# Performance work log

Measured on AMD Instinct MI355X. Metric: run time of the kernel, lower is better.

The kernel has to match this reference:

```python
import jax, jax.numpy as jnp
import numpy as np

N_NODES = 100000
N_EDGES = 1600000
NFEAT = 128
NHID = 128
NS = 64
NCLASS = 16
B = 8192


def setup_inputs() -> dict:
    key = jax.random.key(0)
    ks = jax.random.split(key, 12)
    s = jax.random.normal(ks[0], (B, NS), dtype=jnp.float32)
    x = jax.random.normal(ks[1], (N_NODES, NFEAT), dtype=jnp.float32)
    row = jax.random.randint(ks[2], (N_EDGES,), 0, N_NODES)
    col = jax.random.randint(ks[3], (N_EDGES,), 0, N_NODES)
    val = jax.random.uniform(ks[4], (N_EDGES,), dtype=jnp.float32)
    index = jax.random.randint(ks[5], (B,), 0, N_NODES)
    # learned parameters (glorot-ish scale)
    W1 = jax.random.normal(ks[6], (NFEAT, NHID), dtype=jnp.float32) / np.sqrt(NFEAT)
    b1 = jnp.zeros((NHID,), dtype=jnp.float32)
    W2 = jax.random.normal(ks[7], (NHID, NHID), dtype=jnp.float32) / np.sqrt(NHID)
    b2 = jnp.zeros((NHID,), dtype=jnp.float32)
    Wl = jax.random.normal(ks[8], (NHID + NS, NCLASS), dtype=jnp.float32) / np.sqrt(NHID + NS)
    bl = jnp.zeros((NCLASS,), dtype=jnp.float32)
    return {"s": s, "x": x, "row": row, "col": col, "val": val,
            "index": index, "W1": W1, "b1": b1, "W2": W2, "b2": b2,
            "Wl": Wl, "bl": bl}


def reference(s, x, row, col, val, index, W1, b1, W2, b2, Wl, bl):
    n = x.shape[0]

    def spmm(h):
        # adj @ h with adj in COO form: out[r] += val_e * h[c]
        return jax.ops.segment_sum(val[:, None] * h[col], row, num_segments=n)

    # dropout is identity in eval mode (training=False)
    h = jax.nn.relu(spmm(x @ W1) + b1)          # gc1 + relu
    h = spmm(h @ W2) + b2                        # gc2
    z = jnp.concatenate([h[index], s], axis=1) @ Wl + bl  # [B, nclass]
    return jax.nn.log_softmax(z, axis=1)
```

## Files before the change

kernel.cpp:

```cpp
#include <hip/hip_runtime.h>
#include <math.h>

#define N_NODES 100000
#define N_EDGES 1600000
#define NFEAT 128
#define NHID 128
#define NS 64
#define NCLASS 16
#define BB 8192

#define B1_SHIFT 11
#define NB1 49
#define SUB_SHIFT 5
#define NSUB 3125
#define CHUNKA 2048
#define HWG 256
#define BINC_CAP 2048

typedef unsigned long long ull;
typedef unsigned int uint;


__device__ __forceinline__ unsigned short f2bf(float f) {
  unsigned int u = __float_as_uint(f);
  return (unsigned short)((u + 0x7fffu + ((u >> 16) & 1u)) >> 16);
}
__device__ __forceinline__ float bflo(unsigned int u) {
  return __uint_as_float(u << 16);
}
__device__ __forceinline__ float bfhi(unsigned int u) {
  return __uint_as_float(u & 0xffff0000u);
}
__device__ __forceinline__ unsigned int packbf2(float lo, float hi) {
  return (unsigned int)f2bf(lo) | ((unsigned int)f2bf(hi) << 16);
}


__device__ __forceinline__ ull pack_edge(float v, int r, int c) {
  return ((ull)(__float_as_uint(v) >> 2) << 34) | ((ull)(unsigned)r << 17) | (unsigned)c;
}
__device__ __forceinline__ int edge_col(ull p) { return (int)(p & 0x1FFFFu); }
__device__ __forceinline__ int edge_row(ull p) { return (int)((unsigned)(p >> 17) & 0x1FFFFu); }
__device__ __forceinline__ float edge_val(ull p) {
  return __uint_as_float(((unsigned)(p >> 34)) << 2);
}


__global__ __launch_bounds__(256) void selbuild_kernel(const int* __restrict__ index,
                                                       int* __restrict__ sel) {
  int t = blockIdx.x * 256 + threadIdx.x;
  sel[index[t]] = 1;
}

__global__ __launch_bounds__(256) void selflag_kernel(const int* __restrict__ row,
                                                      const int* __restrict__ col,
                                                      const int* __restrict__ sel,
                                                      int* __restrict__ flag) {
  int i = blockIdx.x * blockDim.x + threadIdx.x;
  int stride = gridDim.x * blockDim.x;
  for (; i < N_EDGES; i += stride)
    if (sel[row[i]]) flag[col[i]] = 1;
}

__global__ __launch_bounds__(256) void keepbits_kernel(const int* __restrict__ flag,
                                                       const int* __restrict__ sel,
                                                       uint* __restrict__ keepbits) {
  int t = blockIdx.x * 256 + threadIdx.x;
  if (t >= NSUB) return;
  uint w = 0;
  int base = t * 32;
#pragma unroll
  for (int k = 0; k < 32; ++k) {
    int r = base + k;
    if (r < N_NODES && (flag[r] | sel[r])) w |= (1u << k);
  }
  keepbits[t] = w;
}


__global__ __launch_bounds__(256) void histsub_kernel(const int* __restrict__ row,
                                                      const uint* __restrict__ keepbits,
                                                      int* __restrict__ subcnt) {
  __shared__ int lh[NSUB];
  int tid = threadIdx.x;
  for (int i = tid; i < NSUB; i += 256) lh[i] = 0;
  __syncthreads();
  for (long i = (long)blockIdx.x * 256 + tid; i < N_EDGES; i += (long)HWG * 256) {
    int r = row[i];
    if ((keepbits[r >> 5] >> (r & 31)) & 1u) atomicAdd(&lh[r >> SUB_SHIFT], 1);
  }
  __syncthreads();
  for (int i = tid; i < NSUB; i += 256) {
    int c = lh[i];
    if (c) atomicAdd(&subcnt[i], c);
  }
}


__global__ __launch_bounds__(1024) void scanall_kernel(const int* __restrict__ subcnt,
                                                       int* __restrict__ sub_offs,
                                                       int* __restrict__ gcur1,
                                                       int* __restrict__ gcur2) {
  __shared__ int sd[1024];
  int tid = threadIdx.x;
  int b0 = tid * 4;
  int vv[4];
  int loc = 0;
#pragma unroll
  for (int k = 0; k < 4; ++k) {
    int i = b0 + k;
    vv[k] = (i < NSUB) ? subcnt[i] : 0;
    loc += vv[k];
  }
  sd[tid] = loc;
  __syncthreads();
  for (int o = 1; o < 1024; o <<= 1) {
    int add = (tid >= o) ? sd[tid - o] : 0;
    __syncthreads();
    sd[tid] += add;
    __syncthreads();
  }
  int pre = sd[tid] - loc;
#pragma unroll
  for (int k = 0; k < 4; ++k) {
    int i = b0 + k;
    if (i < NSUB) {
      sub_offs[i] = pre;
      gcur2[i] = pre;
      if ((i & 63) == 0) gcur1[i >> 6] = pre;
      pre += vv[k];
    }
  }
  if (tid == 1023) sub_offs[NSUB] = sd[1023];
}


__global__ __launch_bounds__(256) void binA_kernel(const int* __restrict__ row,
                                                   const int* __restrict__ col,
                                                   const float* __restrict__ val,
                                                   const uint* __restrict__ keepbits,
                                                   int* __restrict__ gcur1,
                                                   ull* __restrict__ ebuf1) {
  __shared__ ull stage[CHUNKA];
  __shared__ short bkt[CHUNKA];
  __shared__ int hist[NB1], lofs[NB1 + 1], lcur[NB1], gbase[NB1];
  int tid = threadIdx.x;
  for (long base = (long)blockIdx.x * CHUNKA; base < N_EDGES; base += (long)gridDim.x * CHUNKA) {
    int cnt = (int)min((long)CHUNKA, (long)N_EDGES - base);
    if (tid < NB1) hist[tid] = 0;
    __syncthreads();
    ull e[8]; int bk[8];
#pragma unroll
    for (int v = 0; v < 8; ++v) {
      int i = v * 256 + tid;
      bk[v] = -1;
      if (i < cnt) {
        long g = base + i;
        int r = row[g];
        if ((keepbits[r >> 5] >> (r & 31)) & 1u) {
          e[v] = pack_edge(val[g], r, col[g]);
          bk[v] = r >> B1_SHIFT;
          atomicAdd(&hist[bk[v]], 1);
        }
      }
    }
    __syncthreads();
    if (tid < 64) {
      int h = (tid < NB1) ? hist[tid] : 0;
      int x = h;
      for (int o = 1; o < 64; o <<= 1) {
        int y = __shfl_up(x, o);
        if (tid >= o) x += y;
      }
      if (tid < NB1) { lofs[tid] = x - h; lcur[tid] = x - h; }
      if (tid == 63) lofs[NB1] = x;
    }
    __syncthreads();
#pragma unroll
    for (int v = 0; v < 8; ++v) {
      if (bk[v] >= 0) {
        int pos = atomicAdd(&lcur[bk[v]], 1);
        stage[pos] = e[v];
        bkt[pos] = (short)bk[v];
      }
    }
    __syncthreads();
    if (tid < NB1) {
      int h = hist[tid];
      if (h > 0) gbase[tid] = atomicAdd(&gcur1[tid], h);
    }
    __syncthreads();
    int tot = lofs[NB1];
    for (int s = tid; s < tot; s += 256) {
      int lo = bkt[s];
      ebuf1[gbase[lo] + (s - lofs[lo])] = stage[s];
    }
    __syncthreads();
  }
}


__global__ __launch_bounds__(256) void binB_kernel(const ull* __restrict__ ebuf1,
                                                   const int* __restrict__ sub_offs,
                                                   int* __restrict__ gcur2,
                                                   ull* __restrict__ edat) {
  __shared__ ull stage[CHUNKA];
  __shared__ short bkt[CHUNKA];
  __shared__ int hist[64], lofs[65], lcur[64], gbase[64];
  int tid = threadIdx.x;
  int b1 = blockIdx.x >> 3, w = blockIdx.x & 7;
  int rbeg = sub_offs[b1 << 6];
  int rend = sub_offs[min((b1 + 1) << 6, NSUB)];
  for (int base = rbeg + w * CHUNKA; base < rend; base += 8 * CHUNKA) {
    int cnt = min(CHUNKA, rend - base);
    if (tid < 64) hist[tid] = 0;
    __syncthreads();
    ull e[8]; int bk[8];
#pragma unroll
    for (int v = 0; v < 8; ++v) {
      int i = v * 256 + tid;
      bk[v] = -1;
      if (i < cnt) {
        e[v] = ebuf1[base + i];
        bk[v] = (edge_row(e[v]) >> SUB_SHIFT) - (b1 << 6);
        atomicAdd(&hist[bk[v]], 1);
      }
    }
    __syncthreads();
    if (tid < 64) {
      int h = hist[tid];
      int x = h;
      for (int o = 1; o < 64; o <<= 1) {
        int y = __shfl_up(x, o);
        if (tid >= o) x += y;
      }
      lofs[tid] = x - h;
      lcur[tid] = x - h;
      if (tid == 63) lofs[64] = x;
    }
    __syncthreads();
#pragma unroll
    for (int v = 0; v < 8; ++v) {
      if (bk[v] >= 0) {
        int pos = atomicAdd(&lcur[bk[v]], 1);
        stage[pos] = e[v];
        bkt[pos] = (short)bk[v];
      }
    }
    __syncthreads();
    if (tid < 64) {
      int h = hist[tid];
      if (h > 0) gbase[tid] = atomicAdd(&gcur2[(b1 << 6) + tid], h);
    }
    __syncthreads();
    for (int s = tid; s < cnt; s += 256) {
      int lo = bkt[s];
      edat[gbase[lo] + (s - lofs[lo])] = stage[s];
    }
    __syncthreads();
  }
}


__global__ __launch_bounds__(256) void binC_kernel(const int* __restrict__ sub_offs,
                                                   ull* __restrict__ edat,
                                                   ull* __restrict__ ebuf1,
                                                   int* __restrict__ offs) {
  __shared__ ull es[BINC_CAP];
  __shared__ int rcnt[32], rcur[32];
  int s = blockIdx.x, tid = threadIdx.x;
  int r0 = s << SUB_SHIFT;
  int beg = sub_offs[s], end = sub_offs[s + 1];
  int n = end - beg;
  if (tid < 32) rcnt[tid] = 0;
  __syncthreads();
  if (n <= BINC_CAP) {
    for (int i = tid; i < n; i += 256) {
      ull p = edat[beg + i];
      es[i] = p;
      atomicAdd(&rcnt[edge_row(p) & 31], 1);
    }
    __syncthreads();
    if (tid < 32) {
      int h = rcnt[tid];
      int x = h;
      for (int o = 1; o < 32; o <<= 1) {
        int y = __shfl_up(x, o, 32);
        if (tid >= o) x += y;
      }
      rcur[tid] = x - h;
      offs[r0 + tid] = beg + x - h;
      if (s == NSUB - 1 && tid == 31) offs[N_NODES] = end;
    }
    __syncthreads();
    for (int i = tid; i < n; i += 256) {
      ull p = es[i];
      int pos = atomicAdd(&rcur[edge_row(p) & 31], 1);
      edat[beg + pos] = p;
    }
  } else {
    for (int i = tid; i < n; i += 256) {
      ull p = edat[beg + i];
      ebuf1[beg + i] = p;
      atomicAdd(&rcnt[edge_row(p) & 31], 1);
    }
    __syncthreads();
    if (tid < 32) {
      int h = rcnt[tid];
      int x = h;
      for (int o = 1; o < 32; o <<= 1) {
        int y = __shfl_up(x, o, 32);
        if (tid >= o) x += y;
      }
      rcur[tid] = x - h;
      offs[r0 + tid] = beg + x - h;
      if (s == NSUB - 1 && tid == 31) offs[N_NODES] = end;
    }
    __syncthreads();
    for (int i = tid; i < n; i += 256) {
      ull p = ebuf1[beg + i];
      int pos = atomicAdd(&rcur[edge_row(p) & 31], 1);
      edat[beg + pos] = p;
    }
  }
}


__global__ __launch_bounds__(256) void wconv2_kernel(const float* __restrict__ W1,
                                                     const float* __restrict__ W2,
                                                     uint* __restrict__ Wt1,
                                                     uint* __restrict__ Wt2) {
  int blk = blockIdx.x;
  const float* W = (blk < 32) ? W1 : W2;
  uint* Wt = (blk < 32) ? Wt1 : Wt2;
  int idx = (blk & 31) * 256 + threadIdx.x;
  int n = idx >> 6, kc = idx & 63;
  float lo = W[(2 * kc) * 128 + n];
  float hi = W[(2 * kc + 1) * 128 + n];
  Wt[idx] = packbf2(lo, hi);
}


typedef __attribute__((ext_vector_type(8))) __bf16 bf16x8;
typedef __attribute__((ext_vector_type(4))) float f32x4;
union FragU { uint4 u; bf16x8 b; };

#define LDSTR 68

template <int OUT_BF16>
__global__ __launch_bounds__(256) void mfma_gemm_kernel(const float* __restrict__ A,
                                                        const uint* __restrict__ Wt_g,
                                                        const float* __restrict__ bias,
                                                        void* __restrict__ C,
                                                        int nrows) {
  __shared__ uint As_s[64 * LDSTR];
  __shared__ uint Wt_s[128 * LDSTR];
  int tid = threadIdx.x;
  int rbase = blockIdx.x * 64;

  {
    const uint2* src = (const uint2*)Wt_g;
#pragma unroll
    for (int i = 0; i < 16; ++i) {
      int j = i * 256 + tid;
      int n = j >> 5, c2 = (j & 31) * 2;
      uint2 v = src[j];
      Wt_s[n * LDSTR + c2] = v.x;
      Wt_s[n * LDSTR + c2 + 1] = v.y;
    }
  }
  {
    const float4* src = (const float4*)(A + (long)rbase * 128);
#pragma unroll
    for (int i = 0; i < 8; ++i) {
      int f = i * 256 + tid;
      int m = f >> 5;
      float4 v = (rbase + m < nrows) ? src[f] : make_float4(0.f, 0.f, 0.f, 0.f);
      int c = (f & 31) * 2;
      As_s[m * LDSTR + c]     = packbf2(v.x, v.y);
      As_s[m * LDSTR + c + 1] = packbf2(v.z, v.w);
    }
  }
  __syncthreads();

  int w = tid >> 6, lane = tid & 63;
  int quad = lane >> 4, lr = lane & 15;
  int n0 = w * 32;

  f32x4 acc[4][2];
#pragma unroll
  for (int mt = 0; mt < 4; ++mt)
#pragma unroll
    for (int nt = 0; nt < 2; ++nt) acc[mt][nt] = (f32x4){0.f, 0.f, 0.f, 0.f};

#pragma unroll
  for (int kk = 0; kk < 4; ++kk) {
    int kc = kk * 16 + quad * 4;
    FragU fb0, fb1;
    fb0.u = *(const uint4*)&Wt_s[(n0 + lr) * LDSTR + kc];
    fb1.u = *(const uint4*)&Wt_s[(n0 + 16 + lr) * LDSTR + kc];
#pragma unroll
    for (int mt = 0; mt < 4; ++mt) {
      FragU fa;
      fa.u = *(const uint4*)&As_s[(mt * 16 + lr) * LDSTR + kc];
      acc[mt][0] = __builtin_amdgcn_mfma_f32_16x16x32_bf16(fa.b, fb0.b, acc[mt][0], 0, 0, 0);
      acc[mt][1] = __builtin_amdgcn_mfma_f32_16x16x32_bf16(fa.b, fb1.b, acc[mt][1], 0, 0, 0);
    }
  }

#pragma unroll
  for (int mt = 0; mt < 4; ++mt) {
#pragma unroll
    for (int nt = 0; nt < 2; ++nt) {
      int col = n0 + nt * 16 + lr;
      float bv = OUT_BF16 ? 0.f : bias[col];
#pragma unroll
      for (int r = 0; r < 4; ++r) {
        int row = rbase + mt * 16 + quad * 4 + r;
        if (row < nrows) {
          if (OUT_BF16)
            ((unsigned short*)C)[(long)row * 128 + col] = f2bf(acc[mt][nt][r]);
          else
            ((float*)C)[(long)row * 128 + col] = acc[mt][nt][r] + bv;
        }
      }
    }
  }
}


__device__ __forceinline__ void fma_row(float* acc, float v, uint4 u) {
  acc[0] = fmaf(v, bflo(u.x), acc[0]);
  acc[1] = fmaf(v, bfhi(u.x), acc[1]);
  acc[2] = fmaf(v, bflo(u.y), acc[2]);
  acc[3] = fmaf(v, bfhi(u.y), acc[3]);
  acc[4] = fmaf(v, bflo(u.z), acc[4]);
  acc[5] = fmaf(v, bfhi(u.z), acc[5]);
  acc[6] = fmaf(v, bflo(u.w), acc[6]);
  acc[7] = fmaf(v, bfhi(u.w), acc[7]);
}

__global__ __launch_bounds__(256) void spmm_row_kernel(const int* __restrict__ offs,
                                                       const ull* __restrict__ edat,
                                                       const unsigned short* __restrict__ a,
                                                       const float* __restrict__ bias,
                                                       unsigned short* __restrict__ h,
                                                       const int* __restrict__ flag) {
  int wave = threadIdx.x >> 6;
  int lane = threadIdx.x & 63;
  int r = blockIdx.x * 4 + wave;
  if (!flag[r]) return;
  int g = lane >> 4, l = lane & 15;
  int s = offs[r], e = offs[r + 1];
  float acc[8] = {0.f, 0.f, 0.f, 0.f, 0.f, 0.f, 0.f, 0.f};
  int j = s + g;
  for (; j + 4 < e; j += 8) {
    ull p0 = edat[j];
    ull p1 = edat[j + 4];
    uint4 u0 = *(const uint4*)(a + (long)edge_col(p0) * 128 + l * 8);
    uint4 u1 = *(const uint4*)(a + (long)edge_col(p1) * 128 + l * 8);
    fma_row(acc, edge_val(p0), u0);
    fma_row(acc, edge_val(p1), u1);
  }
  if (j < e) {
    ull p = edat[j];
    uint4 u = *(const uint4*)(a + (long)edge_col(p) * 128 + l * 8);
    fma_row(acc, edge_val(p), u);
  }
#pragma unroll
  for (int k = 0; k < 8; ++k) {
    acc[k] += __shfl_xor(acc[k], 16);
    acc[k] += __shfl_xor(acc[k], 32);
  }
  if (g == 0) {
    float4 b0 = *(const float4*)(bias + l * 8);
    float4 b1 = *(const float4*)(bias + l * 8 + 4);
    uint4 o;
    o.x = packbf2(fmaxf(acc[0] + b0.x, 0.f), fmaxf(acc[1] + b0.y, 0.f));
    o.y = packbf2(fmaxf(acc[2] + b0.z, 0.f), fmaxf(acc[3] + b0.w, 0.f));
    o.z = packbf2(fmaxf(acc[4] + b1.x, 0.f), fmaxf(acc[5] + b1.y, 0.f));
    o.w = packbf2(fmaxf(acc[6] + b1.z, 0.f), fmaxf(acc[7] + b1.w, 0.f));
    *(uint4*)(h + (long)r * 128 + l * 8) = o;
  }
}

__global__ __launch_bounds__(256) void spmm_sel_kernel(const int* __restrict__ offs,
                                                       const ull* __restrict__ edat,
                                                       const unsigned short* __restrict__ h1,
                                                       const int* __restrict__ index,
                                                       float* __restrict__ g2) {
  int wave = threadIdx.x >> 6;
  int lane = threadIdx.x & 63;
  int b = blockIdx.x * 4 + wave;
  int g = lane >> 4, l = lane & 15;
  int r = index[b];
  int s = offs[r], e = offs[r + 1];
  float acc[8] = {0.f, 0.f, 0.f, 0.f, 0.f, 0.f, 0.f, 0.f};
  int j = s + g;
  for (; j + 4 < e; j += 8) {
    ull p0 = edat[j];
    ull p1 = edat[j + 4];
    uint4 u0 = *(const uint4*)(h1 + (long)edge_col(p0) * 128 + l * 8);
    uint4 u1 = *(const uint4*)(h1 + (long)edge_col(p1) * 128 + l * 8);
    fma_row(acc, edge_val(p0), u0);
    fma_row(acc, edge_val(p1), u1);
  }
  if (j < e) {
    ull p = edat[j];
    uint4 u = *(const uint4*)(h1 + (long)edge_col(p) * 128 + l * 8);
    fma_row(acc, edge_val(p), u);
  }
#pragma unroll
  for (int k = 0; k < 8; ++k) {
    acc[k] += __shfl_xor(acc[k], 16);
    acc[k] += __shfl_xor(acc[k], 32);
  }
  if (g == 0) {
    float* op = g2 + (long)b * 128 + l * 8;
    *(float4*)(op + 0) = make_float4(acc[0], acc[1], acc[2], acc[3]);
    *(float4*)(op + 4) = make_float4(acc[4], acc[5], acc[6], acc[7]);
  }
}


__global__ __launch_bounds__(128) void final_kernel(const float* __restrict__ t,
                                                    const float* __restrict__ s,
                                                    const float* __restrict__ Wl,
                                                    const float* __restrict__ bl,
                                                    float* __restrict__ out) {
  int b = blockIdx.x * 128 + threadIdx.x;
  float z[16];
#pragma unroll
  for (int c = 0; c < 16; ++c) z[c] = bl[c];
  const float4* tb = (const float4*)(t + (long)b * 128);
#pragma unroll 4
  for (int k4 = 0; k4 < 32; ++k4) {
    float4 tv = tb[k4];
    const float* w = Wl + (k4 * 4) * 16;
#pragma unroll
    for (int c = 0; c < 16; ++c)
      z[c] += tv.x * w[c] + tv.y * w[16 + c] + tv.z * w[32 + c] + tv.w * w[48 + c];
  }
  const float4* sb = (const float4*)(s + (long)b * 64);
#pragma unroll 4
  for (int k4 = 0; k4 < 16; ++k4) {
    float4 sv = sb[k4];
    const float* w = Wl + (128 + k4 * 4) * 16;
#pragma unroll
    for (int c = 0; c < 16; ++c)
      z[c] += sv.x * w[c] + sv.y * w[16 + c] + sv.z * w[32 + c] + sv.w * w[48 + c];
  }
  float m = z[0];
#pragma unroll
  for (int c = 1; c < 16; ++c) m = fmaxf(m, z[c]);
  float sum = 0.f;
#pragma unroll
  for (int c = 0; c < 16; ++c) sum += expf(z[c] - m);
  float lse = m + logf(sum);
  float* ob = out + (long)b * 16;
#pragma unroll
  for (int c = 0; c < 16; ++c) ob[c] = z[c] - lse;
}


extern "C" void kernel_launch(void* const* d_in, const int* in_sizes, int n_in,
                              void* d_out, int out_size, void* d_ws, size_t ws_size,
                              hipStream_t stream) {
  const float* s_in  = (const float*)d_in[0];
  const float* x     = (const float*)d_in[1];
  const int*   row   = (const int*)d_in[2];
  const int*   col   = (const int*)d_in[3];
  const float* val   = (const float*)d_in[4];
  const int*   index = (const int*)d_in[5];
  const float* W1    = (const float*)d_in[6];
  const float* b1    = (const float*)d_in[7];
  const float* W2    = (const float*)d_in[8];
  const float* b2    = (const float*)d_in[9];
  const float* Wl    = (const float*)d_in[10];
  const float* bl    = (const float*)d_in[11];
  float* out = (float*)d_out;

  ull* edat  = (ull*)d_ws;
  ull* ebuf1 = edat + N_EDGES;
  unsigned short* a  = (unsigned short*)(ebuf1 + N_EDGES);
  unsigned short* h1 = a + (size_t)N_NODES * 128;
  float* g2   = (float*)(h1 + (size_t)N_NODES * 128);
  float* tmat = g2 + (size_t)BB * 128;
  int* flag   = (int*)(tmat + (size_t)BB * 128);
  int* sel    = flag + N_NODES;
  int* subcnt = sel + N_NODES;
  int* offs   = subcnt + NSUB;
  int* sub_offs = offs + (N_NODES + 1);
  int* gcur1  = sub_offs + (NSUB + 1);
  int* gcur2  = gcur1 + NB1;
  uint* keepbits = (uint*)(gcur2 + NSUB);
  uint* Wt1   = keepbits + NSUB;
  uint* Wt2   = Wt1 + 8192;

  hipMemsetAsync(flag, 0, (2 * N_NODES + NSUB) * sizeof(int), stream);

  selbuild_kernel<<<BB / 256, 256, 0, stream>>>(index, sel);
  selflag_kernel<<<4096, 256, 0, stream>>>(row, col, sel, flag);
  keepbits_kernel<<<(NSUB + 255) / 256, 256, 0, stream>>>(flag, sel, keepbits);

  histsub_kernel<<<HWG, 256, 0, stream>>>(row, keepbits, subcnt);
  scanall_kernel<<<1, 1024, 0, stream>>>(subcnt, sub_offs, gcur1, gcur2);

  binA_kernel<<<512, 256, 0, stream>>>(row, col, val, keepbits, gcur1, ebuf1);
  binB_kernel<<<NB1 * 8, 256, 0, stream>>>(ebuf1, sub_offs, gcur2, edat);
  binC_kernel<<<NSUB, 256, 0, stream>>>(sub_offs, edat, ebuf1, offs);

  wconv2_kernel<<<64, 256, 0, stream>>>(W1, W2, Wt1, Wt2);

  mfma_gemm_kernel<1><<<(N_NODES + 63) / 64, 256, 0, stream>>>(x, Wt1, nullptr, a, N_NODES);
  spmm_row_kernel<<<N_NODES / 4, 256, 0, stream>>>(offs, edat, a, b1, h1, flag);
  spmm_sel_kernel<<<BB / 4, 256, 0, stream>>>(offs, edat, h1, index, g2);
  mfma_gemm_kernel<0><<<BB / 64, 256, 0, stream>>>(g2, Wt2, b2, tmat, BB);
  final_kernel<<<BB / 128, 128, 0, stream>>>(tmat, s_in, Wl, bl, out);
}
```

Before: 307.1 us.

## Build keep bitmask via atomicOr and fuse GEMM2 with final log-softmax layer

Replaces the flag array and keepbits pass with direct atomicOr into a bitmask during selection. Removes the separate weight-conversion kernel by converting W1/W2 to bf16 inside each GEMM block. Fuses the second GEMM with the classifier and log_softmax through shared memory, dropping the intermediate tmat buffer. This removes several launches and a global round-trip, but every GEMM1 block now redundantly reads and converts W1, and spmm_row now also processes selected rows.

```diff
diff --git a/kernel.cpp b/kernel.cpp
--- a/kernel.cpp
+++ b/kernel.cpp
@@ -44,42 +44,36 @@
 __device__ __forceinline__ float edge_val(ull p) {
   return __uint_as_float(((unsigned)(p >> 34)) << 2);
 }
+__device__ __forceinline__ int keep_test(const uint* keep, int r) {
+  return (keep[r >> 5] >> (r & 31)) & 1u;
+}
 
 
 __global__ __launch_bounds__(256) void selbuild_kernel(const int* __restrict__ index,
-                                                       int* __restrict__ sel) {
+                                                       int* __restrict__ sel,
+                                                       uint* __restrict__ keep) {
   int t = blockIdx.x * 256 + threadIdx.x;
-  sel[index[t]] = 1;
+  int r = index[t];
+  sel[r] = 1;
+  atomicOr(&keep[r >> 5], 1u << (r & 31));
 }
 
 __global__ __launch_bounds__(256) void selflag_kernel(const int* __restrict__ row,
                                                       const int* __restrict__ col,
                                                       const int* __restrict__ sel,
-                                                      int* __restrict__ flag) {
+                                                      uint* __restrict__ keep) {
   int i = blockIdx.x * blockDim.x + threadIdx.x;
   int stride = gridDim.x * blockDim.x;
   for (; i < N_EDGES; i += stride)
-    if (sel[row[i]]) flag[col[i]] = 1;
-}
-
-__global__ __launch_bounds__(256) void keepbits_kernel(const int* __restrict__ flag,
-                                                       const int* __restrict__ sel,
-                                                       uint* __restrict__ keepbits) {
-  int t = blockIdx.x * 256 + threadIdx.x;
-  if (t >= NSUB) return;
-  uint w = 0;
-  int base = t * 32;
-#pragma unroll
-  for (int k = 0; k < 32; ++k) {
-    int r = base + k;
-    if (r < N_NODES && (flag[r] | sel[r])) w |= (1u << k);
-  }
-  keepbits[t] = w;
+    if (sel[row[i]]) {
+      int c = col[i];
+      atomicOr(&keep[c >> 5], 1u << (c & 31));
+    }
 }
 
 
 __global__ __launch_bounds__(256) void histsub_kernel(const int* __restrict__ row,
-                                                      const uint* __restrict__ keepbits,
+                                                      const uint* __restrict__ keep,
                                                       int* __restrict__ subcnt) {
   __shared__ int lh[NSUB];
   int tid = threadIdx.x;
@@ -87,7 +81,7 @@
   __syncthreads();
   for (long i = (long)blockIdx.x * 256 + tid; i < N_EDGES; i += (long)HWG * 256) {
     int r = row[i];
-    if ((keepbits[r >> 5] >> (r & 31)) & 1u) atomicAdd(&lh[r >> SUB_SHIFT], 1);
+    if (keep_test(keep, r)) atomicAdd(&lh[r >> SUB_SHIFT], 1);
   }
   __syncthreads();
   for (int i = tid; i < NSUB; i += 256) {
@@ -138,7 +132,7 @@
 __global__ __launch_bounds__(256) void binA_kernel(const int* __restrict__ row,
                                                    const int* __restrict__ col,
                                                    const float* __restrict__ val,
-                                                   const uint* __restrict__ keepbits,
+                                                   const uint* __restrict__ keep,
                                                    int* __restrict__ gcur1,
                                                    ull* __restrict__ ebuf1) {
   __shared__ ull stage[CHUNKA];
@@ -157,7 +151,7 @@
       if (i < cnt) {
         long g = base + i;
         int r = row[g];
-        if ((keepbits[r >> 5] >> (r & 31)) & 1u) {
+        if (keep_test(keep, r)) {
           e[v] = pack_edge(val[g], r, col[g]);
           bk[v] = r >> B1_SHIFT;
           atomicAdd(&hist[bk[v]], 1);
@@ -326,47 +320,27 @@
 }
 
 
-__global__ __launch_bounds__(256) void wconv2_kernel(const float* __restrict__ W1,
-                                                     const float* __restrict__ W2,
-                                                     uint* __restrict__ Wt1,
-                                                     uint* __restrict__ Wt2) {
-  int blk = blockIdx.x;
-  const float* W = (blk < 32) ? W1 : W2;
-  uint* Wt = (blk < 32) ? Wt1 : Wt2;
-  int idx = (blk & 31) * 256 + threadIdx.x;
-  int n = idx >> 6, kc = idx & 63;
-  float lo = W[(2 * kc) * 128 + n];
-  float hi = W[(2 * kc + 1) * 128 + n];
-  Wt[idx] = packbf2(lo, hi);
-}
-
-
 typedef __attribute__((ext_vector_type(8))) __bf16 bf16x8;
 typedef __attribute__((ext_vector_type(4))) float f32x4;
 union FragU { uint4 u; bf16x8 b; };
 
 #define LDSTR 68
 
-template <int OUT_BF16>
-__global__ __launch_bounds__(256) void mfma_gemm_kernel(const float* __restrict__ A,
-                                                        const uint* __restrict__ Wt_g,
-                                                        const float* __restrict__ bias,
-                                                        void* __restrict__ C,
-                                                        int nrows) {
+__global__ __launch_bounds__(256) void gemm1_kernel(const float* __restrict__ A,
+                                                    const float* __restrict__ W,
+                                                    unsigned short* __restrict__ C,
+                                                    int nrows) {
   __shared__ uint As_s[64 * LDSTR];
   __shared__ uint Wt_s[128 * LDSTR];
   int tid = threadIdx.x;
   int rbase = blockIdx.x * 64;
 
   {
-    const uint2* src = (const uint2*)Wt_g;
-#pragma unroll
-    for (int i = 0; i < 16; ++i) {
-      int j = i * 256 + tid;
-      int n = j >> 5, c2 = (j & 31) * 2;
-      uint2 v = src[j];
-      Wt_s[n * LDSTR + c2] = v.x;
-      Wt_s[n * LDSTR + c2 + 1] = v.y;
+    int n = tid & 127, hh = tid >> 7;
+#pragma unroll
+    for (int kk = 0; kk < 32; ++kk) {
+      int kc = hh * 32 + kk;
+      Wt_s[n * LDSTR + kc] = packbf2(W[(2 * kc) * 128 + n], W[(2 * kc + 1) * 128 + n]);
     }
   }
   {
@@ -413,18 +387,126 @@
 #pragma unroll
     for (int nt = 0; nt < 2; ++nt) {
       int col = n0 + nt * 16 + lr;
-      float bv = OUT_BF16 ? 0.f : bias[col];
 #pragma unroll
       for (int r = 0; r < 4; ++r) {
         int row = rbase + mt * 16 + quad * 4 + r;
-        if (row < nrows) {
-          if (OUT_BF16)
-            ((unsigned short*)C)[(long)row * 128 + col] = f2bf(acc[mt][nt][r]);
-          else
-            ((float*)C)[(long)row * 128 + col] = acc[mt][nt][r] + bv;
-        }
-      }
-    }
+        if (row < nrows) C[(long)row * 128 + col] = f2bf(acc[mt][nt][r]);
+      }
+    }
+  }
+}
+
+
+__global__ __launch_bounds__(256) void gemm2f_kernel(const float* __restrict__ g2,
+                                                     const float* __restrict__ W2,
+                                                     const float* __restrict__ b2,
+                                                     const float* __restrict__ s_in,
+                                                     const float* __restrict__ Wl,
+                                                     const float* __restrict__ bl,
+                                                     float* __restrict__ out) {
+  __shared__ uint smem[13056];
+  uint* Wt_s = smem;
+  uint* As_s = smem + 128 * LDSTR;
+  float* ts  = (float*)smem;
+  float* Wls = (float*)(smem + 128 * LDSTR);
+  int tid = threadIdx.x;
+  int rbase = blockIdx.x * 64;
+
+  {
+    int n = tid & 127, hh = tid >> 7;
+#pragma unroll
+    for (int kk = 0; kk < 32; ++kk) {
+      int kc = hh * 32 + kk;
+      Wt_s[n * LDSTR + kc] = packbf2(W2[(2 * kc) * 128 + n], W2[(2 * kc + 1) * 128 + n]);
+    }
+  }
+  {
+    const float4* src = (const float4*)(g2 + (long)rbase * 128);
+#pragma unroll
+    for (int i = 0; i < 8; ++i) {
+      int f = i * 256 + tid;
+      int m = f >> 5, c = (f & 31) * 2;
+      float4 v = src[f];
+      As_s[m * LDSTR + c]     = packbf2(v.x, v.y);
+      As_s[m * LDSTR + c + 1] = packbf2(v.z, v.w);
+    }
+  }
+  __syncthreads();
+
+  int w = tid >> 6, lane = tid & 63;
+  int quad = lane >> 4, lr = lane & 15;
+  int n0 = w * 32;
+
+  f32x4 acc[4][2];
+#pragma unroll
+  for (int mt = 0; mt < 4; ++mt)
+#pragma unroll
+    for (int nt = 0; nt < 2; ++nt) acc[mt][nt] = (f32x4){0.f, 0.f, 0.f, 0.f};
+
+#pragma unroll
+  for (int kk = 0; kk < 4; ++kk) {
+    int kc = kk * 16 + quad * 4;
+    FragU fb0, fb1;
+    fb0.u = *(const uint4*)&Wt_s[(n0 + lr) * LDSTR + kc];
+    fb1.u = *(const uint4*)&Wt_s[(n0 + 16 + lr) * LDSTR + kc];
+#pragma unroll
+    for (int mt = 0; mt < 4; ++mt) {
+      FragU fa;
+      fa.u = *(const uint4*)&As_s[(mt * 16 + lr) * LDSTR + kc];
+      acc[mt][0] = __builtin_amdgcn_mfma_f32_16x16x32_bf16(fa.b, fb0.b, acc[mt][0], 0, 0, 0);
+      acc[mt][1] = __builtin_amdgcn_mfma_f32_16x16x32_bf16(fa.b, fb1.b, acc[mt][1], 0, 0, 0);
+    }
+  }
+  __syncthreads();
+
+#pragma unroll
+  for (int mt = 0; mt < 4; ++mt) {
+#pragma unroll
+    for (int nt = 0; nt < 2; ++nt) {
+      int col = n0 + nt * 16 + lr;
+      float bv = b2[col];
+#pragma unroll
+      for (int r = 0; r < 4; ++r)
+        ts[(mt * 16 + quad * 4 + r) * 129 + col] = acc[mt][nt][r] + bv;
+    }
+  }
+  for (int i = tid; i < 192 * 16; i += 256) Wls[i] = Wl[i];
+  __syncthreads();
+
+  int q = lane & 3;
+  int mrow = w * 16 + (lane >> 2);
+  int b = rbase + mrow;
+  float z[16];
+#pragma unroll
+  for (int c = 0; c < 16; ++c) z[c] = 0.f;
+  int k0 = q * 48;
+  for (int kk = 0; kk < 48; ++kk) {
+    int k = k0 + kk;
+    float xv = (k < 128) ? ts[mrow * 129 + k] : s_in[(long)b * 64 + (k - 128)];
+    const float* wp = Wls + k * 16;
+#pragma unroll
+    for (int c = 0; c < 16; ++c) z[c] = fmaf(xv, wp[c], z[c]);
+  }
+#pragma unroll
+  for (int c = 0; c < 16; ++c) {
+    z[c] += __shfl_xor(z[c], 1);
+    z[c] += __shfl_xor(z[c], 2);
+  }
+  if (q == 0) {
+#pragma unroll
+    for (int c = 0; c < 16; ++c) z[c] += bl[c];
+    float mx = z[0];
+#pragma unroll
+    for (int c = 1; c < 16; ++c) mx = fmaxf(mx, z[c]);
+    float sum = 0.f;
+#pragma unroll
+    for (int c = 0; c < 16; ++c) sum += expf(z[c] - mx);
+    float lse = mx + logf(sum);
+    float4* ob = (float4*)(out + (long)b * 16);
+    ob[0] = make_float4(z[0] - lse, z[1] - lse, z[2] - lse, z[3] - lse);
+    ob[1] = make_float4(z[4] - lse, z[5] - lse, z[6] - lse, z[7] - lse);
+    ob[2] = make_float4(z[8] - lse, z[9] - lse, z[10] - lse, z[11] - lse);
+    ob[3] = make_float4(z[12] - lse, z[13] - lse, z[14] - lse, z[15] - lse);
   }
 }
 
@@ -445,11 +527,11 @@
                                                        const unsigned short* __restrict__ a,
                                                        const float* __restrict__ bias,
                                                        unsigned short* __restrict__ h,
-                                                       const int* __restrict__ flag) {
+                                                       const uint* __restrict__ keep) {
   int wave = threadIdx.x >> 6;
   int lane = threadIdx.x & 63;
   int r = blockIdx.x * 4 + wave;
-  if (!flag[r]) return;
+  if (!keep_test(keep, r)) return;
   int g = lane >> 4, l = lane & 15;
   int s = offs[r], e = offs[r + 1];
   float acc[8] = {0.f, 0.f, 0.f, 0.f, 0.f, 0.f, 0.f, 0.f};
@@ -523,46 +605,6 @@
 }
 
 
-__global__ __launch_bounds__(128) void final_kernel(const float* __restrict__ t,
-                                                    const float* __restrict__ s,
-                                                    const float* __restrict__ Wl,
-                                                    const float* __restrict__ bl,
-                                                    float* __restrict__ out) {
-  int b = blockIdx.x * 128 + threadIdx.x;
-  float z[16];
-#pragma unroll
-  for (int c = 0; c < 16; ++c) z[c] = bl[c];
-  const float4* tb = (const float4*)(t + (long)b * 128);
-#pragma unroll 4
-  for (int k4 = 0; k4 < 32; ++k4) {
-    float4 tv = tb[k4];
-    const float* w = Wl + (k4 * 4) * 16;
-#pragma unroll
-    for (int c = 0; c < 16; ++c)
-      z[c] += tv.x * w[c] + tv.y * w[16 + c] + tv.z * w[32 + c] + tv.w * w[48 + c];
-  }
-  const float4* sb = (const float4*)(s + (long)b * 64);
-#pragma unroll 4
-  for (int k4 = 0; k4 < 16; ++k4) {
-    float4 sv = sb[k4];
-    const float* w = Wl + (128 + k4 * 4) * 16;
-#pragma unroll
-    for (int c = 0; c < 16; ++c)
-      z[c] += sv.x * w[c] + sv.y * w[16 + c] + sv.z * w[32 + c] + sv.w * w[48 + c];
-  }
-  float m = z[0];
-#pragma unroll
-  for (int c = 1; c < 16; ++c) m = fmaxf(m, z[c]);
-  float sum = 0.f;
-#pragma unroll
-  for (int c = 0; c < 16; ++c) sum += expf(z[c] - m);
-  float lse = m + logf(sum);
-  float* ob = out + (long)b * 16;
-#pragma unroll
-  for (int c = 0; c < 16; ++c) ob[c] = z[c] - lse;
-}
-
-
 extern "C" void kernel_launch(void* const* d_in, const int* in_sizes, int n_in,
                               void* d_out, int out_size, void* d_ws, size_t ws_size,
                               hipStream_t stream) {
@@ -585,36 +627,27 @@
   unsigned short* a  = (unsigned short*)(ebuf1 + N_EDGES);
   unsigned short* h1 = a + (size_t)N_NODES * 128;
   float* g2   = (float*)(h1 + (size_t)N_NODES * 128);
-  float* tmat = g2 + (size_t)BB * 128;
-  int* flag   = (int*)(tmat + (size_t)BB * 128);
-  int* sel    = flag + N_NODES;
+  int* sel    = (int*)(g2 + (size_t)BB * 128);
   int* subcnt = sel + N_NODES;
-  int* offs   = subcnt + NSUB;
+  uint* keep  = (uint*)(subcnt + NSUB);
+  int* offs   = (int*)(keep + NSUB);
   int* sub_offs = offs + (N_NODES + 1);
   int* gcur1  = sub_offs + (NSUB + 1);
   int* gcur2  = gcur1 + NB1;
-  uint* keepbits = (uint*)(gcur2 + NSUB);
-  uint* Wt1   = keepbits + NSUB;
-  uint* Wt2   = Wt1 + 8192;
-
-  hipMemsetAsync(flag, 0, (2 * N_NODES + NSUB) * sizeof(int), stream);
-
-  selbuild_kernel<<<BB / 256, 256, 0, stream>>>(index, sel);
-  selflag_kernel<<<4096, 256, 0, stream>>>(row, col, sel, flag);
-  keepbits_kernel<<<(NSUB + 255) / 256, 256, 0, stream>>>(flag, sel, keepbits);
-
-  histsub_kernel<<<HWG, 256, 0, stream>>>(row, keepbits, subcnt);
+
+  hipMemsetAsync(sel, 0, (N_NODES + 2 * NSUB) * sizeof(int), stream);
+
+  selbuild_kernel<<<BB / 256, 256, 0, stream>>>(index, sel, keep);
+  selflag_kernel<<<4096, 256, 0, stream>>>(row, col, sel, keep);
+  histsub_kernel<<<HWG, 256, 0, stream>>>(row, keep, subcnt);
   scanall_kernel<<<1, 1024, 0, stream>>>(subcnt, sub_offs, gcur1, gcur2);
 
-  binA_kernel<<<512, 256, 0, stream>>>(row, col, val, keepbits, gcur1, ebuf1);
+  binA_kernel<<<512, 256, 0, stream>>>(row, col, val, keep, gcur1, ebuf1);
   binB_kernel<<<NB1 * 8, 256, 0, stream>>>(ebuf1, sub_offs, gcur2, edat);
   binC_kernel<<<NSUB, 256, 0, stream>>>(sub_offs, edat, ebuf1, offs);
 
-  wconv2_kernel<<<64, 256, 0, stream>>>(W1, W2, Wt1, Wt2);
-
-  mfma_gemm_kernel<1><<<(N_NODES + 63) / 64, 256, 0, stream>>>(x, Wt1, nullptr, a, N_NODES);
-  spmm_row_kernel<<<N_NODES / 4, 256, 0, stream>>>(offs, edat, a, b1, h1, flag);
+  gemm1_kernel<<<(N_NODES + 63) / 64, 256, 0, stream>>>(x, W1, a, N_NODES);
+  spmm_row_kernel<<<N_NODES / 4, 256, 0, stream>>>(offs, edat, a, b1, h1, keep);
   spmm_sel_kernel<<<BB / 4, 256, 0, stream>>>(offs, edat, h1, index, g2);
-  mfma_gemm_kernel<0><<<BB / 64, 256, 0, stream>>>(g2, Wt2, b2, tmat, BB);
-  final_kernel<<<BB / 128, 128, 0, stream>>>(tmat, s_in, Wl, bl, out);
-}
+  gemm2f_kernel<<<BB / 64, 256, 0, stream>>>(g2, W2, b2, s_in, Wl, bl, out);
+}
```

New measurement: 299.2 us. 1.03x faster.
